# Kernel optimization log

Measured on AMD Instinct MI355X. Metric: run time of the kernel, lower is better.

## Reference

```python
import jax, jax.numpy as jnp
import numpy as np

WINDOW = 128
CAUSAL = True
LOOK_BACKWARD = 1
LOOK_FORWARD = 0  # causal forces look_forward = 0


def _look_around(x, backward, forward, pad_value, dim):
    # pad along window axis (axis=1), then concat shifted slices along `dim`
    nw = x.shape[1]
    pad_cfg = [(0, 0)] * x.ndim
    pad_cfg[1] = (backward, forward)
    padded = jnp.pad(x, pad_cfg, constant_values=pad_value)
    slices = [padded[:, i:i + nw] for i in range(forward + backward + 1)]
    return jnp.concatenate(slices, axis=dim)


def setup_inputs() -> dict:
    key = jax.random.key(0)
    kq, kk, kv = jax.random.split(key, 3)
    shape = (2, 16, 4096, 64)
    return {
        "q": jax.random.normal(kq, shape, dtype=jnp.float32),
        "k": jax.random.normal(kk, shape, dtype=jnp.float32),
        "v": jax.random.normal(kv, shape, dtype=jnp.float32),
    }


def reference(q, k, v):
    b, h, t, e = q.shape
    scale = e ** (-0.5)
    windows = t // WINDOW  # t assumed divisible by WINDOW (pad_to_multiple is no-op)

    # merge batch and heads, bucket into windows
    bq = q.reshape(b * h, windows, WINDOW, e)
    bk = k.reshape(b * h, windows, WINDOW, e)
    bv = v.reshape(b * h, windows, WINDOW, e)

    # look-around gather of key/value windows: j-dim = WINDOW*(1+back+fwd)
    bk = _look_around(bk, LOOK_BACKWARD, LOOK_FORWARD, 0.0, dim=2)
    bv = _look_around(bv, LOOK_BACKWARD, LOOK_FORWARD, 0.0, dim=2)

    # positional indices for masking
    bq_t = jnp.arange(t).reshape(1, windows, WINDOW)
    bq_k = _look_around(bq_t, LOOK_BACKWARD, LOOK_FORWARD, -1, dim=2)

    mask = (bq_k == -1)[:, :, None, :]  # (1, w, 1, j) padded positions
    if CAUSAL:
        mask = mask | (bq_t[:, :, :, None] < bq_k[:, :, None, :])

    dots = jnp.einsum('bwie,bwje->bwij', bq * scale, bk)
    mask_value = -jnp.finfo(dots.dtype).max
    dots = jnp.where(mask, mask_value, dots)
    attn = jax.nn.softmax(dots.astype(jnp.float32), axis=-1).astype(dots.dtype)
    out = jnp.einsum('bwij,bwje->bwie', attn, bv)
    return out.reshape(b, h, t, e)
```

## Files before the change

### kernel.cpp

```cpp
#include <hip/hip_runtime.h>

#define T_DIM 4096
#define E_DIM 64
#define WIN   128
#define NWIN  (T_DIM / WIN)
#define VT_LD 136

typedef __bf16  bf16x8 __attribute__((ext_vector_type(8)));
typedef float   f32x16 __attribute__((ext_vector_type(16)));

__global__ __launch_bounds__(256, 4)
void la_fwd(const float* __restrict__ Q, const float* __restrict__ K,
            const float* __restrict__ V, float* __restrict__ O)
{
  __shared__ __align__(16) __bf16 Vt0[E_DIM * VT_LD];
  __shared__ __align__(16) __bf16 Vt1[E_DIM * VT_LD];

  const int tid  = threadIdx.x;
  const int lane = tid & 63;
  const int wid  = tid >> 6;
  const int col  = lane & 31;
  const int half = lane >> 5;

  const int w  = blockIdx.x;
  const int bh = blockIdx.y;

  const float* Qb = Q + (size_t)bh * T_DIM * E_DIM;
  const float* Kb = K + (size_t)bh * T_DIM * E_DIM;
  const float* Vb = V + (size_t)bh * T_DIM * E_DIM;
  float*       Ob = O + (size_t)bh * T_DIM * E_DIM;

  const int q0 = w * WIN;

  auto stage = [&](int kr0, __bf16* Vt) {
    const int j  = tid & 127;
    const int ch = (tid >> 7) * 32;
    const float* vrow = Vb + (size_t)(kr0 + j) * E_DIM + ch;
#pragma unroll
    for (int c4 = 0; c4 < 8; ++c4) {
      const float4 vv = *(const float4*)(vrow + c4 * 4);
      const int e = ch + c4 * 4;
      Vt[(e + 0) * VT_LD + j] = (__bf16)vv.x;
      Vt[(e + 1) * VT_LD + j] = (__bf16)vv.y;
      Vt[(e + 2) * VT_LD + j] = (__bf16)vv.z;
      Vt[(e + 3) * VT_LD + j] = (__bf16)vv.w;
    }
  };
  if (w > 0) stage(q0 - WIN, Vt0);
  stage(q0, Vt1);

  const float QS = 0.125f * 1.44269504088896340736f;
  bf16x8 bq[4];
  {
    const float* qrow = Qb + (size_t)(q0 + wid * 32 + col) * E_DIM;
#pragma unroll
    for (int c = 0; c < 4; ++c) {
      const float* p = qrow + c * 16 + half * 8;
      const float4 x = *(const float4*)(p);
      const float4 y = *(const float4*)(p + 4);
      bf16x8 a;
      a[0]=(__bf16)(x.x*QS); a[1]=(__bf16)(x.y*QS); a[2]=(__bf16)(x.z*QS); a[3]=(__bf16)(x.w*QS);
      a[4]=(__bf16)(y.x*QS); a[5]=(__bf16)(y.y*QS); a[6]=(__bf16)(y.z*QS); a[7]=(__bf16)(y.w*QS);
      bq[c] = a;
    }
  }

  float  lsum = 0.0f;
  f32x16 oacc[2];
#pragma unroll
  for (int et = 0; et < 2; ++et)
#pragma unroll
    for (int r = 0; r < 16; ++r) oacc[et][r] = 0.0f;

  __syncthreads();

  auto kb_step = [&](const float* krows, const __bf16* Vt, int kbj0, bool diag) {
    f32x16 s;
#pragma unroll
    for (int r = 0; r < 16; ++r) s[r] = 0.0f;
#pragma unroll
    for (int c = 0; c < 4; ++c) {
      const float* p = krows + (size_t)col * E_DIM + c * 16 + half * 8;
      const float4 x = *(const float4*)(p);
      const float4 y = *(const float4*)(p + 4);
      bf16x8 a;
      a[0]=(__bf16)x.x; a[1]=(__bf16)x.y; a[2]=(__bf16)x.z; a[3]=(__bf16)x.w;
      a[4]=(__bf16)y.x; a[5]=(__bf16)y.y; a[6]=(__bf16)y.z; a[7]=(__bf16)y.w;
      s = __builtin_amdgcn_mfma_f32_32x32x16_bf16(a, bq[c], s, 0, 0, 0);
    }
    float pr[16];
#pragma unroll
    for (int r = 0; r < 16; ++r) {
      const int key = (r & 3) + 8 * (r >> 2) + 4 * half;
      float sv = s[r];
      if (diag && key > col) sv = -3.0e38f;
      const float p = __builtin_amdgcn_exp2f(sv);
      lsum += p;
      pr[r] = p;
    }
#pragma unroll
    for (int g = 0; g < 2; ++g) {
      int A0, A1, B0, B1;
      asm("v_cvt_pk_bf16_f32 %0, %1, %2" : "=v"(A0) : "v"(pr[8*g+0]), "v"(pr[8*g+1]));
      asm("v_cvt_pk_bf16_f32 %0, %1, %2" : "=v"(A1) : "v"(pr[8*g+2]), "v"(pr[8*g+3]));
      asm("v_cvt_pk_bf16_f32 %0, %1, %2" : "=v"(B0) : "v"(pr[8*g+4]), "v"(pr[8*g+5]));
      asm("v_cvt_pk_bf16_f32 %0, %1, %2" : "=v"(B1) : "v"(pr[8*g+6]), "v"(pr[8*g+7]));
      asm("v_permlane32_swap_b32 %0, %1" : "+v"(A0), "+v"(B0));
      asm("v_permlane32_swap_b32 %0, %1" : "+v"(A1), "+v"(B1));
      union { int d[4]; bf16x8 v; } u;
      u.d[0] = A0; u.d[1] = A1; u.d[2] = B0; u.d[3] = B1;
      const int j0 = kbj0 + g * 16 + half * 8;
#pragma unroll
      for (int et = 0; et < 2; ++et) {
        const bf16x8 bv = *(const bf16x8*)(&Vt[(et * 32 + col) * VT_LD + j0]);
        oacc[et] = __builtin_amdgcn_mfma_f32_32x32x16_bf16(u.v, bv, oacc[et], 0, 0, 0);
      }
    }
  };

  if (w > 0) {
    const float* kp = Kb + (size_t)(q0 - WIN) * E_DIM;
#pragma unroll
    for (int kb = 0; kb < 4; ++kb)
      kb_step(kp + (size_t)kb * 32 * E_DIM, Vt0, kb * 32, false);
  }

  {
    const float* kp = Kb + (size_t)q0 * E_DIM;
#pragma unroll
    for (int kb = 0; kb < 4; ++kb)
      if (kb <= wid) kb_step(kp + (size_t)kb * 32 * E_DIM, Vt1, kb * 32, kb == wid);
  }

  float xx = lsum, yy = lsum;
  asm("v_permlane32_swap_b32 %0, %1" : "+v"(xx), "+v"(yy));
  const float ltot = xx + yy;
#pragma unroll
  for (int r = 0; r < 16; ++r) {
    const int row = (r & 3) + 8 * (r >> 2) + 4 * half;
    const float lq   = __int_as_float(__builtin_amdgcn_ds_bpermute(row << 2, __float_as_int(ltot)));
    const float rinv = __builtin_amdgcn_rcpf(lq);
    float* op = Ob + (size_t)(q0 + wid * 32 + row) * E_DIM;
    op[col]      = oacc[0][r] * rinv;
    op[col + 32] = oacc[1][r] * rinv;
  }
}

extern "C" void kernel_launch(void* const* d_in, const int* in_sizes, int n_in,
                              void* d_out, int out_size, void* d_ws, size_t ws_size,
                              hipStream_t stream) {
  const float* Q = (const float*)d_in[0];
  const float* K = (const float*)d_in[1];
  const float* V = (const float*)d_in[2];
  float*       O = (float*)d_out;
  const int bh = in_sizes[0] / (T_DIM * E_DIM);
  dim3 grid(NWIN, bh);
  la_fwd<<<grid, 256, 0, stream>>>(Q, K, V, O);
}
```

Before: 152.9 us.

## Stage K through LDS, batch all global loads upfront, coalesce output via LDS

All K, V and Q global loads are issued together at kernel start into registers. K is converted once to bf16 and stored in a shared LDS tile, so waves no longer redundantly load and convert K rows from global memory in every step. V is transposed with vector LDS writes. The output is staged through LDS and written as coalesced float4 stores. In exchange LDS use grows to about 52KB and register pressure rises, so occupancy drops to 3 blocks per CU, and extra barriers are added between the two key windows.

```diff
diff --git a/kernel.cpp b/kernel.cpp
--- a/kernel.cpp
+++ b/kernel.cpp
@@ -4,17 +4,23 @@
 #define E_DIM 64
 #define WIN   128
 #define NWIN  (T_DIM / WIN)
+#define KS_LD 72
 #define VT_LD 136
-
+#define OS_LD 68
+
+typedef __bf16  bf16x4 __attribute__((ext_vector_type(4)));
 typedef __bf16  bf16x8 __attribute__((ext_vector_type(8)));
 typedef float   f32x16 __attribute__((ext_vector_type(16)));
 
-__global__ __launch_bounds__(256, 4)
+__global__ __launch_bounds__(256, 3)
 void la_fwd(const float* __restrict__ Q, const float* __restrict__ K,
             const float* __restrict__ V, float* __restrict__ O)
 {
-  __shared__ __align__(16) __bf16 Vt0[E_DIM * VT_LD];
-  __shared__ __align__(16) __bf16 Vt1[E_DIM * VT_LD];
+  __shared__ __align__(16) unsigned char lds_raw[53248];
+  __bf16* Ks  = (__bf16*)(lds_raw);
+  __bf16* Vt0 = (__bf16*)(lds_raw + 18432);
+  __bf16* Vt1 = (__bf16*)(lds_raw + 35840);
+  float*  Os  = (float*)(lds_raw);
 
   const int tid  = threadIdx.x;
   const int lane = tid & 63;
@@ -31,39 +37,87 @@
   float*       Ob = O + (size_t)bh * T_DIM * E_DIM;
 
   const int q0 = w * WIN;
-
-  auto stage = [&](int kr0, __bf16* Vt) {
-    const int j  = tid & 127;
-    const int ch = (tid >> 7) * 32;
-    const float* vrow = Vb + (size_t)(kr0 + j) * E_DIM + ch;
-#pragma unroll
-    for (int c4 = 0; c4 < 8; ++c4) {
-      const float4 vv = *(const float4*)(vrow + c4 * 4);
-      const int e = ch + c4 * 4;
-      Vt[(e + 0) * VT_LD + j] = (__bf16)vv.x;
-      Vt[(e + 1) * VT_LD + j] = (__bf16)vv.y;
-      Vt[(e + 2) * VT_LD + j] = (__bf16)vv.z;
-      Vt[(e + 3) * VT_LD + j] = (__bf16)vv.w;
-    }
-  };
-  if (w > 0) stage(q0 - WIN, Vt0);
-  stage(q0, Vt1);
+  const int e0 = (tid & 15) << 2;
+  const int jb = (tid >> 4) << 2;
+
+  const float* kp1 = Kb + (size_t)q0 * E_DIM;
+  const float* vp1 = Vb + (size_t)q0 * E_DIM;
+  const float* kp0 = kp1 - WIN * E_DIM;
+  const float* vp0 = vp1 - WIN * E_DIM;
+
+  float4 k0f[8], v0f[8], k1f[8], v1f[8], qf[8];
+  if (w > 0) {
+#pragma unroll
+    for (int i = 0; i < 8; ++i) k0f[i] = *(const float4*)(kp0 + (i << 10) + (tid << 2));
+#pragma unroll
+    for (int p = 0; p < 2; ++p)
+#pragma unroll
+      for (int r = 0; r < 4; ++r)
+        v0f[p * 4 + r] = *(const float4*)(vp0 + (size_t)(p * 64 + jb + r) * E_DIM + e0);
+  }
+#pragma unroll
+  for (int i = 0; i < 8; ++i) k1f[i] = *(const float4*)(kp1 + (i << 10) + (tid << 2));
+#pragma unroll
+  for (int p = 0; p < 2; ++p)
+#pragma unroll
+    for (int r = 0; r < 4; ++r)
+      v1f[p * 4 + r] = *(const float4*)(vp1 + (size_t)(p * 64 + jb + r) * E_DIM + e0);
+  {
+    const float* qrow = Qb + (size_t)(q0 + wid * 32 + col) * E_DIM;
+#pragma unroll
+    for (int c = 0; c < 4; ++c) {
+      qf[2 * c]     = *(const float4*)(qrow + c * 16 + half * 8);
+      qf[2 * c + 1] = *(const float4*)(qrow + c * 16 + half * 8 + 4);
+    }
+  }
+
+  auto cvt8 = [&](const float4* src, bf16x4* dst) {
+#pragma unroll
+    for (int i = 0; i < 8; ++i) {
+      const float* f = (const float*)&src[i];
+      bf16x4 b;
+      b[0] = (__bf16)f[0]; b[1] = (__bf16)f[1]; b[2] = (__bf16)f[2]; b[3] = (__bf16)f[3];
+      dst[i] = b;
+    }
+  };
+  bf16x4 k0b[8], v0b[8], k1b[8], v1b[8];
+  if (w > 0) { cvt8(k0f, k0b); cvt8(v0f, v0b); }
+  cvt8(k1f, k1b); cvt8(v1f, v1b);
 
   const float QS = 0.125f * 1.44269504088896340736f;
   bf16x8 bq[4];
-  {
-    const float* qrow = Qb + (size_t)(q0 + wid * 32 + col) * E_DIM;
-#pragma unroll
-    for (int c = 0; c < 4; ++c) {
-      const float* p = qrow + c * 16 + half * 8;
-      const float4 x = *(const float4*)(p);
-      const float4 y = *(const float4*)(p + 4);
-      bf16x8 a;
-      a[0]=(__bf16)(x.x*QS); a[1]=(__bf16)(x.y*QS); a[2]=(__bf16)(x.z*QS); a[3]=(__bf16)(x.w*QS);
-      a[4]=(__bf16)(y.x*QS); a[5]=(__bf16)(y.y*QS); a[6]=(__bf16)(y.z*QS); a[7]=(__bf16)(y.w*QS);
-      bq[c] = a;
-    }
-  }
+#pragma unroll
+  for (int c = 0; c < 4; ++c) {
+    const float* x = (const float*)&qf[2 * c];
+    const float* y = (const float*)&qf[2 * c + 1];
+    bf16x8 a;
+    a[0]=(__bf16)(x[0]*QS); a[1]=(__bf16)(x[1]*QS); a[2]=(__bf16)(x[2]*QS); a[3]=(__bf16)(x[3]*QS);
+    a[4]=(__bf16)(y[0]*QS); a[5]=(__bf16)(y[1]*QS); a[6]=(__bf16)(y[2]*QS); a[7]=(__bf16)(y[3]*QS);
+    bq[c] = a;
+  }
+
+  auto writeK = [&](const bf16x4* ksrc) {
+#pragma unroll
+    for (int i = 0; i < 8; ++i) {
+      const int fi = (i << 10) + (tid << 2);
+      *(bf16x4*)(&Ks[(fi >> 6) * KS_LD + (fi & 63)]) = ksrc[i];
+    }
+  };
+  auto writeV = [&](const bf16x4* vsrc, __bf16* Vt) {
+#pragma unroll
+    for (int p = 0; p < 2; ++p)
+#pragma unroll
+      for (int c = 0; c < 4; ++c) {
+        bf16x4 t;
+        t[0] = vsrc[p*4+0][c]; t[1] = vsrc[p*4+1][c];
+        t[2] = vsrc[p*4+2][c]; t[3] = vsrc[p*4+3][c];
+        *(bf16x4*)(&Vt[(e0 + c) * VT_LD + p * 64 + jb]) = t;
+      }
+  };
+
+  if (w > 0) { writeK(k0b); writeV(v0b, Vt0); }
+  else       { writeK(k1b); }
+  writeV(v1b, Vt1);
 
   float  lsum = 0.0f;
   f32x16 oacc[2];
@@ -74,18 +128,13 @@
 
   __syncthreads();
 
-  auto kb_step = [&](const float* krows, const __bf16* Vt, int kbj0, bool diag) {
+  auto kb_step = [&](const __bf16* Vt, int kb, bool diag) {
     f32x16 s;
 #pragma unroll
     for (int r = 0; r < 16; ++r) s[r] = 0.0f;
 #pragma unroll
     for (int c = 0; c < 4; ++c) {
-      const float* p = krows + (size_t)col * E_DIM + c * 16 + half * 8;
-      const float4 x = *(const float4*)(p);
-      const float4 y = *(const float4*)(p + 4);
-      bf16x8 a;
-      a[0]=(__bf16)x.x; a[1]=(__bf16)x.y; a[2]=(__bf16)x.z; a[3]=(__bf16)x.w;
-      a[4]=(__bf16)y.x; a[5]=(__bf16)y.y; a[6]=(__bf16)y.z; a[7]=(__bf16)y.w;
+      const bf16x8 a = *(const bf16x8*)(&Ks[(kb * 32 + col) * KS_LD + c * 16 + half * 8]);
       s = __builtin_amdgcn_mfma_f32_32x32x16_bf16(a, bq[c], s, 0, 0, 0);
     }
     float pr[16];
@@ -109,7 +158,7 @@
       asm("v_permlane32_swap_b32 %0, %1" : "+v"(A1), "+v"(B1));
       union { int d[4]; bf16x8 v; } u;
       u.d[0] = A0; u.d[1] = A1; u.d[2] = B0; u.d[3] = B1;
-      const int j0 = kbj0 + g * 16 + half * 8;
+      const int j0 = kb * 32 + g * 16 + half * 8;
 #pragma unroll
       for (int et = 0; et < 2; ++et) {
         const bf16x8 bv = *(const bf16x8*)(&Vt[(et * 32 + col) * VT_LD + j0]);
@@ -119,30 +168,38 @@
   };
 
   if (w > 0) {
-    const float* kp = Kb + (size_t)(q0 - WIN) * E_DIM;
-#pragma unroll
-    for (int kb = 0; kb < 4; ++kb)
-      kb_step(kp + (size_t)kb * 32 * E_DIM, Vt0, kb * 32, false);
-  }
-
-  {
-    const float* kp = Kb + (size_t)q0 * E_DIM;
-#pragma unroll
-    for (int kb = 0; kb < 4; ++kb)
-      if (kb <= wid) kb_step(kp + (size_t)kb * 32 * E_DIM, Vt1, kb * 32, kb == wid);
-  }
+#pragma unroll
+    for (int kb = 0; kb < 4; ++kb) kb_step(Vt0, kb, false);
+    __syncthreads();
+    writeK(k1b);
+    __syncthreads();
+  }
+#pragma unroll
+  for (int kb = 0; kb < 4; ++kb)
+    if (kb <= wid) kb_step(Vt1, kb, kb == wid);
 
   float xx = lsum, yy = lsum;
   asm("v_permlane32_swap_b32 %0, %1" : "+v"(xx), "+v"(yy));
   const float ltot = xx + yy;
+
+  __syncthreads();
 #pragma unroll
   for (int r = 0; r < 16; ++r) {
     const int row = (r & 3) + 8 * (r >> 2) + 4 * half;
     const float lq   = __int_as_float(__builtin_amdgcn_ds_bpermute(row << 2, __float_as_int(ltot)));
     const float rinv = __builtin_amdgcn_rcpf(lq);
-    float* op = Ob + (size_t)(q0 + wid * 32 + row) * E_DIM;
-    op[col]      = oacc[0][r] * rinv;
-    op[col + 32] = oacc[1][r] * rinv;
+    Os[(wid * 32 + row) * OS_LD + col]      = oacc[0][r] * rinv;
+    Os[(wid * 32 + row) * OS_LD + col + 32] = oacc[1][r] * rinv;
+  }
+  __syncthreads();
+  {
+    float* ob = Ob + (size_t)q0 * E_DIM;
+#pragma unroll
+    for (int i = 0; i < 8; ++i) {
+      const int fi = (i << 10) + (tid << 2);
+      const float4 o4 = *(const float4*)(&Os[(fi >> 6) * OS_LD + (fi & 63)]);
+      *(float4*)(ob + fi) = o4;
+    }
   }
 }
 
```

After: 136.5 us. 10.7% less time.
